# Kernel tuning notes

Hardware: AMD Instinct MI355X
Metric: run time of the kernel (lower is better)

The kernel has to match this reference:

```python
import jax, jax.numpy as jnp
import numpy as np
import math

B, S, D, H, DK, FF, L = 4, 1024, 512, 8, 64, 2048, 4
IN, NS, SD, TOPK = 768, 4, 64, 2


def _ln(x, g, b, eps=1e-5):
    mu = jnp.mean(x, -1, keepdims=True)
    var = jnp.mean((x - mu) ** 2, -1, keepdims=True)
    return (x - mu) / jnp.sqrt(var + eps) * g + b


def _pos_emb(s, d):
    pos = jnp.arange(s, dtype=jnp.float32)[:, None]
    div = jnp.exp(jnp.arange(0, d, 2, dtype=jnp.float32) * (-math.log(10000.0) / d))
    pe = jnp.zeros((s, d), jnp.float32)
    pe = pe.at[:, 0::2].set(jnp.sin(pos * div))
    pe = pe.at[:, 1::2].set(jnp.cos(pos * div))
    return pe


def setup_inputs() -> dict:
    key = jax.random.key(0)
    ks = iter(jax.random.split(key, 40))
    r = lambda *sh: jax.random.normal(next(ks), sh, jnp.float32)
    p = lambda *sh: jax.random.normal(next(ks), sh, jnp.float32) * 0.02
    inp = {
        'q_raw_seq': r(B, S, NS, IN),
        'm_seq': r(B, S, SD),
        'qa_embed': r(B, S, D),
        # MoE expert FFNs: Linear(IN,IN) -> ReLU -> Linear(IN,D)
        'exp_w1': p(NS, IN, IN), 'exp_b1': jnp.zeros((NS, IN)),
        'exp_w2': p(NS, IN, D), 'exp_b2': jnp.zeros((NS, D)),
        # router input adapter Linear(NS*IN, D)
        'adapt_w': p(NS * IN, D), 'adapt_b': jnp.zeros((D,)),
        'gate_w': p(D + SD, NS), 'gate_b': jnp.zeros((NS,)),
        'moe_ln_g': jnp.ones((D,)), 'moe_ln_b': jnp.zeros((D,)),
        # transformer blocks (kq_same=1 -> k_linear shared for q and k)
        'kw': p(L, D, D), 'kb': jnp.zeros((L, D)),
        'vw': p(L, D, D), 'vb': jnp.zeros((L, D)),
        'ow': p(L, D, D), 'ob': jnp.zeros((L, D)),
        'ln1_g': jnp.ones((L, D)), 'ln1_b': jnp.zeros((L, D)),
        'ff_w1': p(L, D, FF), 'ff_b1': jnp.zeros((L, FF)),
        'ff_w2': p(L, FF, D), 'ff_b2': jnp.zeros((L, D)),
        'ln2_g': jnp.ones((L, D)), 'ln2_b': jnp.zeros((L, D)),
    }
    return inp


def _forward(q_raw_seq, m_seq, qa_embed, exp_w1, exp_b1, exp_w2, exp_b2,
             adapt_w, adapt_b, gate_w, gate_b, moe_ln_g, moe_ln_b,
             kw, kb, vw, vb, ow, ob, ln1_g, ln1_b,
             ff_w1, ff_b1, ff_w2, ff_b2, ln2_g, ln2_b):
    # ---- PolyaParallelMoE (eval: no noise/dropout), has_stages=True ----
    h1 = jax.nn.relu(jnp.einsum('bske,kef->bskf', q_raw_seq, exp_w1) + exp_b1[None, None])
    experts = jnp.einsum('bskf,kfm->bskm', h1, exp_w2) + exp_b2[None, None]  # [B,S,4,D]
    q_flat = q_raw_seq.reshape(q_raw_seq.shape[0], q_raw_seq.shape[1], NS * IN)
    summary = jax.nn.relu(q_flat @ adapt_w + adapt_b)
    logits = jnp.concatenate([summary, m_seq], -1) @ gate_w + gate_b  # [B,S,4]
    top_vals, _ = jax.lax.top_k(logits, TOPK)
    thresh = top_vals[..., -1:]
    masked = jnp.where(logits >= thresh, logits, -jnp.inf)  # scatter top-k, -inf elsewhere
    gate_weights = jax.nn.softmax(masked, -1)
    combined = jnp.einsum('bskm,bsk->bsm', experts, gate_weights)
    q_embed = _ln(combined, moe_ln_g, moe_ln_b)

    # ---- Architecture: positional add + causal transformer blocks ----
    pe = _pos_emb(S, D)
    x = q_embed + pe
    y = qa_embed + pe
    allow = jnp.tril(jnp.ones((S, S), bool), -1)  # strict lower: np.triu(k=0)==0
    scale = 1.0 / math.sqrt(DK)
    for i in range(L):
        kh = (x @ kw[i] + kb[i]).reshape(B, S, H, DK).transpose(0, 2, 1, 3)
        vh = (y @ vw[i] + vb[i]).reshape(B, S, H, DK).transpose(0, 2, 1, 3)
        # kq_same: q = k_linear(query), query==key==x -> qh == kh
        scores = jnp.einsum('bhid,bhjd->bhij', kh, kh) * scale
        scores = jnp.where(allow, scores, -1e32)
        attn = jax.nn.softmax(scores, -1)
        attn = attn.at[:, :, 0, :].set(0.0)  # zero_pad first query row
        ctx = jnp.einsum('bhij,bhjd->bhid', attn, vh).transpose(0, 2, 1, 3).reshape(B, S, D)
        x = _ln(x + (ctx @ ow[i] + ob[i]), ln1_g[i], ln1_b[i])
        ffn = jax.nn.relu(x @ ff_w1[i] + ff_b1[i]) @ ff_w2[i] + ff_b2[i]
        x = _ln(x + ffn, ln2_g[i], ln2_b[i])
        y = x  # after first block, value stream follows torch loop (values=y fixed)
        y = qa_embed + pe  # values stay qa stream per Architecture.forward
    return x


def reference(q_raw_seq, m_seq, qa_embed, exp_w1, exp_b1, exp_w2, exp_b2,
              adapt_w, adapt_b, gate_w, gate_b, moe_ln_g, moe_ln_b,
              kw, kb, vw, vb, ow, ob, ln1_g, ln1_b,
              ff_w1, ff_b1, ff_w2, ff_b2, ln2_g, ln2_b):
    # NOTE: in Architecture.forward, each block is called with query=x, key=x, values=y
    # where y = qa_embed + pe stays fixed across blocks.
    def fwd(*a):
        return _forward(*a)
    return fwd(q_raw_seq, m_seq, qa_embed, exp_w1, exp_b1, exp_w2, exp_b2,
               adapt_w, adapt_b, gate_w, gate_b, moe_ln_g, moe_ln_b,
               kw, kb, vw, vb, ow, ob, ln1_g, ln1_b,
               ff_w1, ff_b1, ff_w2, ff_b2, ln2_g, ln2_b)
```

## Files before the change

kernel.cpp:

```cpp
#include <hip/hip_runtime.h>
#include <hip/hip_bf16.h>

typedef unsigned short u16;
typedef __attribute__((ext_vector_type(8))) short short8;
typedef __attribute__((ext_vector_type(4))) float floatx4;

template <typename T> struct is_u16 { static constexpr bool v = false; };
template <> struct is_u16<u16> { static constexpr bool v = true; };

__device__ __forceinline__ float bf2f(u16 u) {
    unsigned x = (unsigned)u << 16;
    return __uint_as_float(x);
}
__device__ __forceinline__ u16 f2bf(float f) {
    unsigned x = __float_as_uint(f);
    unsigned r = (x + 0x7fffu + ((x >> 16) & 1u)) >> 16;
    return (u16)r;
}

__device__ __forceinline__ float wave_sum(float v) {
    #pragma unroll
    for (int off = 32; off; off >>= 1) v += __shfl_xor(v, off);
    return v;
}

__device__ __forceinline__ void async16(const u16* g, const u16* lds) {
    __builtin_amdgcn_global_load_lds(
        (const __attribute__((address_space(1))) void*)g,
        (__attribute__((address_space(3))) void*)lds, 16, 0, 0);
}

__device__ __forceinline__ void load8f(const float* p, u16* dst) {
    float4 a = *(const float4*)p, b = *(const float4*)(p + 4);
    dst[0] = f2bf(a.x); dst[1] = f2bf(a.y); dst[2] = f2bf(a.z); dst[3] = f2bf(a.w);
    dst[4] = f2bf(b.x); dst[5] = f2bf(b.y); dst[6] = f2bf(b.z); dst[7] = f2bf(b.w);
}

__device__ __forceinline__ void hilo8(const float* p, u16* hi, u16* lo) {
    float4 a = *(const float4*)p, b = *(const float4*)(p + 4);
    float v[8] = {a.x, a.y, a.z, a.w, b.x, b.y, b.z, b.w};
    #pragma unroll
    for (int i = 0; i < 8; ++i) {
        u16 h = f2bf(v[i]);
        hi[i] = h;
        lo[i] = f2bf(v[i] - bf2f(h));
    }
}

__global__ __launch_bounds__(256) void hilo_conv_kernel(
    const float* __restrict__ in, u16* __restrict__ hi, u16* __restrict__ lo)
{
    const size_t i = ((size_t)blockIdx.x * 256 + threadIdx.x) * 8;
    u16 h[8], l[8];
    hilo8(in + i, h, l);
    *(uint4*)&hi[i] = *(const uint4*)h;
    *(uint4*)&lo[i] = *(const uint4*)l;
}

template <typename TA>
__device__ __forceinline__ void gemm_body(
    const TA* __restrict__ A, int lda,
    const u16* __restrict__ Bt, int ldb,
    const float* __restrict__ bias,
    float* __restrict__ Cf, u16* __restrict__ Cb, int ldc,
    int K, int act, int transC)
{
    __shared__ __align__(16) u16 Asm[2 * 128 * 32];
    __shared__ __align__(16) u16 Bsm[2 * 128 * 32];

    const int tid = threadIdx.x;
    const int lane = tid & 63;
    const int wave = tid >> 6;
    const int m0 = blockIdx.y * 128, n0 = blockIdx.x * 128;
    const int wm = (wave >> 1) * 64, wn = (wave & 1) * 64;

    const int r0 = tid >> 2;
    const int kc = (tid & 3) * 8;

    const int kq = (lane >> 4) * 8;
    const int fm = lane & 15;

    const floatx4 zz = {0.f, 0.f, 0.f, 0.f};
    floatx4 acc[4][4];
    #pragma unroll
    for (int mt = 0; mt < 4; ++mt)
        #pragma unroll
        for (int nt = 0; nt < 4; ++nt) acc[mt][nt] = zz;

    const u16* ldsA = Asm + wave * 512;
    const u16* ldsB = Bsm + wave * 512;

    for (int kt = 0; kt < K; kt += 64) {
        if constexpr (is_u16<TA>::v) {
            #pragma unroll
            for (int h = 0; h < 2; ++h) {
                async16(&A[(size_t)(m0 + r0) * lda + kt + h * 32 + kc],      ldsA + h * 4096);
                async16(&A[(size_t)(m0 + r0 + 64) * lda + kt + h * 32 + kc], ldsA + h * 4096 + 2048);
                async16(&Bt[(size_t)(n0 + r0) * ldb + kt + h * 32 + kc],      ldsB + h * 4096);
                async16(&Bt[(size_t)(n0 + r0 + 64) * ldb + kt + h * 32 + kc], ldsB + h * 4096 + 2048);
            }
        } else {
            #pragma unroll
            for (int h = 0; h < 2; ++h) {
                load8f(&A[(size_t)(m0 + r0) * lda + kt + h * 32 + kc],      &Asm[h * 4096 + r0 * 32 + kc]);
                load8f(&A[(size_t)(m0 + r0 + 64) * lda + kt + h * 32 + kc], &Asm[h * 4096 + (r0 + 64) * 32 + kc]);
                *(uint4*)&Bsm[h * 4096 + r0 * 32 + kc]        = *(const uint4*)&Bt[(size_t)(n0 + r0) * ldb + kt + h * 32 + kc];
                *(uint4*)&Bsm[h * 4096 + (r0 + 64) * 32 + kc] = *(const uint4*)&Bt[(size_t)(n0 + r0 + 64) * ldb + kt + h * 32 + kc];
            }
        }
        __syncthreads();

        #pragma unroll
        for (int h = 0; h < 2; ++h) {
            short8 af[4], bfr[4];
            #pragma unroll
            for (int mt = 0; mt < 4; ++mt)
                af[mt] = *(const short8*)&Asm[h * 4096 + (wm + mt * 16 + fm) * 32 + kq];
            #pragma unroll
            for (int nt = 0; nt < 4; ++nt)
                bfr[nt] = *(const short8*)&Bsm[h * 4096 + (wn + nt * 16 + fm) * 32 + kq];

            #pragma unroll
            for (int mt = 0; mt < 4; ++mt)
                #pragma unroll
                for (int nt = 0; nt < 4; ++nt)
                    acc[mt][nt] = __builtin_amdgcn_mfma_f32_16x16x32_bf16(
                        af[mt], bfr[nt], acc[mt][nt], 0, 0, 0);
        }
        __syncthreads();
    }

    const int cr = (lane >> 4) * 4;
    #pragma unroll
    for (int mt = 0; mt < 4; ++mt) {
        #pragma unroll
        for (int nt = 0; nt < 4; ++nt) {
            const int col = n0 + wn + nt * 16 + fm;
            const float bz = bias ? bias[col] : 0.f;
            #pragma unroll
            for (int r = 0; r < 4; ++r) {
                const int row = m0 + wm + mt * 16 + cr + r;
                float v = acc[mt][nt][r] + bz;
                if (act) v = fmaxf(v, 0.f);
                if (Cf) Cf[(size_t)row * ldc + col] = v;
                if (Cb) {
                    if (transC)
                        Cb[(((size_t)(row >> 10) * 512 + col) << 10) + (row & 1023)] = f2bf(v);
                    else
                        Cb[(size_t)row * ldc + col] = f2bf(v);
                }
            }
        }
    }
}

template <typename TA>
__global__ __launch_bounds__(256) void gemm_bf16(
    const TA* __restrict__ A, int lda, long strideAz,
    const u16* __restrict__ Bt, int ldb, long strideBz,
    const float* __restrict__ bias, int strideBiasZ,
    float* __restrict__ Cf, u16* __restrict__ Cb, int ldc, long strideCz,
    int K, int act, int transC)
{
    A += (size_t)blockIdx.z * strideAz;
    Bt += (size_t)blockIdx.z * strideBz;
    if (bias) bias += (size_t)blockIdx.z * strideBiasZ;
    if (Cf) Cf += (size_t)blockIdx.z * strideCz;
    if (Cb) Cb += (size_t)blockIdx.z * strideCz;
    gemm_body<TA>(A, lda, Bt, ldb, bias, Cf, Cb, ldc, K, act, transC);
}

__global__ __launch_bounds__(256) void gemm_kv(
    const u16* __restrict__ xb, const u16* __restrict__ yb,
    const u16* __restrict__ kwt, const u16* __restrict__ vwt,
    const float* __restrict__ kb, const float* __restrict__ vb,
    u16* __restrict__ khb, u16* __restrict__ vhT)
{
    if (blockIdx.z == 0)
        gemm_body<u16>(xb, 512, kwt, 512, kb, nullptr, khb, 512, 512, 0, 0);
    else
        gemm_body<u16>(yb, 512, vwt, 512, vb, nullptr, vhT, 512, 512, 0, 1);
}

__global__ __launch_bounds__(256) void gemm_f32split(
    const u16* __restrict__ Ah, const u16* __restrict__ Al, int lda,
    const u16* __restrict__ Bh, const u16* __restrict__ Bl, int ldb,
    float* __restrict__ Cf, int ldc, long strideCz,
    int kz)
{
    __shared__ __align__(16) u16 Ahs[128 * 32];
    __shared__ __align__(16) u16 Als[128 * 32];
    __shared__ __align__(16) u16 Bhs[128 * 32];
    __shared__ __align__(16) u16 Bls[128 * 32];

    const int tid = threadIdx.x;
    const int lane = tid & 63;
    const int wave = tid >> 6;
    const int m0 = blockIdx.y * 128, n0 = blockIdx.x * 128;
    const int wm = (wave >> 1) * 64, wn = (wave & 1) * 64;
    const int k0 = blockIdx.z * kz;
    Cf += (size_t)blockIdx.z * strideCz;

    const int r0 = tid >> 2;
    const int kc = (tid & 3) * 8;
    const int kq = (lane >> 4) * 8;
    const int fm = lane & 15;

    const floatx4 zz = {0.f, 0.f, 0.f, 0.f};
    floatx4 acc[4][4];
    #pragma unroll
    for (int mt = 0; mt < 4; ++mt)
        #pragma unroll
        for (int nt = 0; nt < 4; ++nt) acc[mt][nt] = zz;

    const u16* ldsAh0 = Ahs + wave * 512;
    const u16* ldsAh1 = Ahs + 2048 + wave * 512;
    const u16* ldsAl0 = Als + wave * 512;
    const u16* ldsAl1 = Als + 2048 + wave * 512;
    const u16* ldsBh0 = Bhs + wave * 512;
    const u16* ldsBh1 = Bhs + 2048 + wave * 512;
    const u16* ldsBl0 = Bls + wave * 512;
    const u16* ldsBl1 = Bls + 2048 + wave * 512;

    for (int kt = 0; kt < kz; kt += 32) {
        const size_t ka = (size_t)(m0 + r0) * lda + k0 + kt + kc;
        const size_t kb = (size_t)(n0 + r0) * ldb + k0 + kt + kc;
        async16(&Ah[ka],                     ldsAh0);
        async16(&Ah[ka + (size_t)64 * lda],  ldsAh1);
        async16(&Al[ka],                     ldsAl0);
        async16(&Al[ka + (size_t)64 * lda],  ldsAl1);
        async16(&Bh[kb],                     ldsBh0);
        async16(&Bh[kb + (size_t)64 * ldb],  ldsBh1);
        async16(&Bl[kb],                     ldsBl0);
        async16(&Bl[kb + (size_t)64 * ldb],  ldsBl1);
        __syncthreads();

        short8 ah[4], al[4], bh[4], bl[4];
        #pragma unroll
        for (int mt = 0; mt < 4; ++mt) {
            ah[mt] = *(const short8*)&Ahs[(wm + mt * 16 + fm) * 32 + kq];
            al[mt] = *(const short8*)&Als[(wm + mt * 16 + fm) * 32 + kq];
        }
        #pragma unroll
        for (int nt = 0; nt < 4; ++nt) {
            bh[nt] = *(const short8*)&Bhs[(wn + nt * 16 + fm) * 32 + kq];
            bl[nt] = *(const short8*)&Bls[(wn + nt * 16 + fm) * 32 + kq];
        }

        #pragma unroll
        for (int mt = 0; mt < 4; ++mt)
            #pragma unroll
            for (int nt = 0; nt < 4; ++nt) {
                acc[mt][nt] = __builtin_amdgcn_mfma_f32_16x16x32_bf16(
                    ah[mt], bh[nt], acc[mt][nt], 0, 0, 0);
                acc[mt][nt] = __builtin_amdgcn_mfma_f32_16x16x32_bf16(
                    al[mt], bh[nt], acc[mt][nt], 0, 0, 0);
                acc[mt][nt] = __builtin_amdgcn_mfma_f32_16x16x32_bf16(
                    ah[mt], bl[nt], acc[mt][nt], 0, 0, 0);
            }
        __syncthreads();
    }

    const int cr = (lane >> 4) * 4;
    #pragma unroll
    for (int mt = 0; mt < 4; ++mt) {
        #pragma unroll
        for (int nt = 0; nt < 4; ++nt) {
            const int col = n0 + wn + nt * 16 + fm;
            #pragma unroll
            for (int r = 0; r < 4; ++r) {
                const int row = m0 + wm + mt * 16 + cr + r;
                Cf[(size_t)row * ldc + col] = acc[mt][nt][r];
            }
        }
    }
}

__global__ __launch_bounds__(64) void gate_fused_kernel(
    const float* __restrict__ ps, const float* __restrict__ adapt_b,
    const float* __restrict__ m_seq,
    const float* __restrict__ gw, const float* __restrict__ gb,
    float* __restrict__ gates)
{
    const int r = blockIdx.x, t = threadIdx.x;
    float p0 = 0.f, p1 = 0.f, p2 = 0.f, p3 = 0.f;
    const float* pr = ps + (size_t)r * 512;
    for (int j = t; j < 512; j += 64) {
        float v = pr[j] + pr[j + 2097152] + pr[j + 4194304] + pr[j + 6291456] + adapt_b[j];
        float s = fmaxf(v, 0.f);
        const float* g = gw + (size_t)j * 4;
        p0 += s * g[0]; p1 += s * g[1]; p2 += s * g[2]; p3 += s * g[3];
    }
    {
        float m = m_seq[(size_t)r * 64 + t];
        const float* g = gw + (size_t)(512 + t) * 4;
        p0 += m * g[0]; p1 += m * g[1]; p2 += m * g[2]; p3 += m * g[3];
    }
    p0 = wave_sum(p0); p1 = wave_sum(p1); p2 = wave_sum(p2); p3 = wave_sum(p3);
    if (t == 0) {
        float lg[4] = { p0 + gb[0], p1 + gb[1], p2 + gb[2], p3 + gb[3] };
        float m1 = -INFINITY, m2 = -INFINITY;
        #pragma unroll
        for (int k = 0; k < 4; ++k) {
            float v = lg[k];
            if (v > m1) { m2 = m1; m1 = v; }
            else if (v > m2) { m2 = v; }
        }
        float wv[4], s = 0.f;
        #pragma unroll
        for (int k = 0; k < 4; ++k) {
            wv[k] = (lg[k] >= m2) ? __expf(lg[k] - m1) : 0.f;
            s += wv[k];
        }
        float inv = 1.f / s;
        #pragma unroll
        for (int k = 0; k < 4; ++k) gates[(size_t)r * 4 + k] = wv[k] * inv;
    }
}

__global__ __launch_bounds__(256) void tconv_kernel(
    const float* __restrict__ in, u16* __restrict__ out, int K, int N)
{
    __shared__ float t[32][33];
    const int n0 = blockIdx.x * 32, k0 = blockIdx.y * 32;
    const size_t bo = (size_t)blockIdx.z * K * N;
    const int tx = threadIdx.x & 31, ty = threadIdx.x >> 5;
    const float* src = in + bo;
    u16* dst = out + bo;
    #pragma unroll
    for (int r = ty; r < 32; r += 8) t[r][tx] = src[(size_t)(k0 + r) * N + n0 + tx];
    __syncthreads();
    #pragma unroll
    for (int r = ty; r < 32; r += 8) dst[(size_t)(n0 + r) * K + k0 + tx] = f2bf(t[tx][r]);
}

__global__ __launch_bounds__(256) void tconv3_kernel(
    const float* __restrict__ kw, const float* __restrict__ vw, const float* __restrict__ ow,
    u16* __restrict__ kwt, u16* __restrict__ vwt, u16* __restrict__ owt)
{
    __shared__ float t[32][33];
    const int z = blockIdx.z;
    const int sel = z >> 2, li = z & 3;
    const float* in = (sel == 0) ? kw : (sel == 1) ? vw : ow;
    u16* outp = (sel == 0) ? kwt : (sel == 1) ? vwt : owt;
    const size_t bo = (size_t)li * 262144;
    const int n0 = blockIdx.x * 32, k0 = blockIdx.y * 32;
    const int tx = threadIdx.x & 31, ty = threadIdx.x >> 5;
    const float* src = in + bo;
    u16* dst = outp + bo;
    #pragma unroll
    for (int r = ty; r < 32; r += 8) t[r][tx] = src[(size_t)(k0 + r) * 512 + n0 + tx];
    __syncthreads();
    #pragma unroll
    for (int r = ty; r < 32; r += 8) dst[(size_t)(n0 + r) * 512 + k0 + tx] = f2bf(t[tx][r]);
}

__global__ __launch_bounds__(256) void tconv_hilo_kernel(
    const float* __restrict__ in, u16* __restrict__ outh, u16* __restrict__ outl,
    int K, int N)
{
    __shared__ float t[32][33];
    const int n0 = blockIdx.x * 32, k0 = blockIdx.y * 32;
    const int tx = threadIdx.x & 31, ty = threadIdx.x >> 5;
    #pragma unroll
    for (int r = ty; r < 32; r += 8) t[r][tx] = in[(size_t)(k0 + r) * N + n0 + tx];
    __syncthreads();
    #pragma unroll
    for (int r = ty; r < 32; r += 8) {
        float v = t[tx][r];
        u16 h = f2bf(v);
        outh[(size_t)(n0 + r) * K + k0 + tx] = h;
        outl[(size_t)(n0 + r) * K + k0 + tx] = f2bf(v - bf2f(h));
    }
}

__global__ void pe_kernel(float* __restrict__ pe)
{
    int idx = blockIdx.x * 256 + threadIdx.x;
    int s = idx >> 9, d = idx & 511;
    float div = expf((float)(d & ~1) * (-9.210340371976184f / 512.0f));
    float ang = (float)s * div;
    pe[idx] = (d & 1) ? cosf(ang) : sinf(ang);
}

__global__ __launch_bounds__(64) void moe_ln_kernel(
    const u16* __restrict__ experts, const float* __restrict__ gates,
    const float* __restrict__ g, const float* __restrict__ bb,
    const float* __restrict__ pe, const float* __restrict__ qa,
    float* __restrict__ x, u16* __restrict__ xb, u16* __restrict__ yb)
{
    const int r = blockIdx.x, t = threadIdx.x;
    const u16* e = experts + (size_t)r * 2048;
    const float g0 = gates[r * 4 + 0], g1 = gates[r * 4 + 1];
    const float g2 = gates[r * 4 + 2], g3 = gates[r * 4 + 3];
    float v[8];
    #pragma unroll
    for (int it = 0; it < 8; ++it) {
        int d = t + it * 64;
        v[it] = g0 * bf2f(e[d]) + g1 * bf2f(e[512 + d])
              + g2 * bf2f(e[1024 + d]) + g3 * bf2f(e[1536 + d]);
    }
    float s = 0.f;
    #pragma unroll
    for (int it = 0; it < 8; ++it) s += v[it];
    s = wave_sum(s);
    const float mu = s * (1.f / 512.f);
    float q = 0.f;
    #pragma unroll
    for (int it = 0; it < 8; ++it) { float dd = v[it] - mu; q += dd * dd; }
    q = wave_sum(q);
    const float rstd = rsqrtf(q * (1.f / 512.f) + 1e-5f);
    const float* per = pe + (size_t)(r & 1023) * 512;
    #pragma unroll
    for (int it = 0; it < 8; ++it) {
        int d = t + it * 64;
        float pv = per[d];
        float o = (v[it] - mu) * rstd * g[d] + bb[d] + pv;
        x[(size_t)r * 512 + d] = o;
        xb[(size_t)r * 512 + d] = f2bf(o);
        yb[(size_t)r * 512 + d] = f2bf(qa[(size_t)r * 512 + d] + pv);
    }
}

__global__ __launch_bounds__(64) void add_ln_kernel(
    float* __restrict__ x, u16* __restrict__ xb,
    const float* __restrict__ t0, const float* __restrict__ t1,
    const float* __restrict__ bias,
    const float* __restrict__ g, const float* __restrict__ bb,
    float* __restrict__ out2)
{
    const int r = blockIdx.x, t = threadIdx.x;
    float* xr = x + (size_t)r * 512;
    float v[8];
    #pragma unroll
    for (int it = 0; it < 8; ++it) {
        int d = t + it * 64;
        float tv = t0[(size_t)r * 512 + d];
        if (t1) tv += t1[(size_t)r * 512 + d];
        if (bias) tv += bias[d];
        v[it] = xr[d] + tv;
    }
    float s = 0.f;
    #pragma unroll
    for (int it = 0; it < 8; ++it) s += v[it];
    s = wave_sum(s);
    const float mu = s * (1.f / 512.f);
    float q = 0.f;
    #pragma unroll
    for (int it = 0; it < 8; ++it) { float dd = v[it] - mu; q += dd * dd; }
    q = wave_sum(q);
    const float rstd = rsqrtf(q * (1.f / 512.f) + 1e-5f);
    #pragma unroll
    for (int it = 0; it < 8; ++it) {
        int d = t + it * 64;
        float o = (v[it] - mu) * rstd * g[d] + bb[d];
        xr[d] = o;
        xb[(size_t)r * 512 + d] = f2bf(o);
        if (out2) out2[(size_t)r * 512 + d] = o;
    }
}

__global__ __launch_bounds__(256) void attn_kernel(
    const u16* __restrict__ kh, const u16* __restrict__ vhT,
    u16* __restrict__ ctx)
{
    __shared__ __align__(16) u16 Qs[64 * 64];
    __shared__ __align__(16) u16 Ks[64 * 64];
    __shared__ __align__(16) u16 Vt[64 * 72];
    __shared__ __align__(16) u16 Ps[64 * 72];

    const int tid = threadIdx.x;
    const int lane = tid & 63, wave = tid >> 6;
    const int quad = lane >> 4, fm = lane & 15;
    const int b = blockIdx.x, h = blockIdx.y;
    const int bz = blockIdx.z;
    const int it = (bz < 8) ? bz : (23 - bz);

    const u16* khb = kh + ((size_t)b * 1024) * 512 + h * 64;
    const u16* vtb = vhT + ((size_t)(b * 512 + h * 64)) * 1024;

    const int lj = tid >> 2;
    const int lc = tid & 3;

    {
        const u16* src = khb + (size_t)(it * 64 + lj) * 512 + lc * 16;
        *(uint4*)&Qs[lj * 64 + lc * 16]     = *(const uint4*)src;
        *(uint4*)&Qs[lj * 64 + lc * 16 + 8] = *(const uint4*)(src + 8);
    }

    const floatx4 zz = {0.f, 0.f, 0.f, 0.f};
    floatx4 o_acc[4];
    #pragma unroll
    for (int nt = 0; nt < 4; ++nt) o_acc[nt] = zz;
    float m_run[4] = { -INFINITY, -INFINITY, -INFINITY, -INFINITY };
    float l_run[4] = {};

    __syncthreads();

    for (int jt = 0; jt <= it; ++jt) {
        {
            const u16* ksrc = khb + (size_t)(jt * 64 + lj) * 512 + lc * 16;
            *(uint4*)&Ks[lj * 64 + lc * 16]     = *(const uint4*)ksrc;
            *(uint4*)&Ks[lj * 64 + lc * 16 + 8] = *(const uint4*)(ksrc + 8);
            const u16* vsrc = vtb + (size_t)lj * 1024 + jt * 64 + lc * 16;
            *(uint4*)&Vt[lj * 72 + lc * 16]     = *(const uint4*)vsrc;
            *(uint4*)&Vt[lj * 72 + lc * 16 + 8] = *(const uint4*)(vsrc + 8);
        }
        __syncthreads();

        floatx4 s_acc[4];
        #pragma unroll
        for (int nt = 0; nt < 4; ++nt) s_acc[nt] = zz;
        #pragma unroll
        for (int ks = 0; ks < 2; ++ks) {
            short8 af = *(const short8*)&Qs[(wave * 16 + fm) * 64 + ks * 32 + quad * 8];
            #pragma unroll
            for (int nt = 0; nt < 4; ++nt) {
                short8 bf = *(const short8*)&Ks[(nt * 16 + fm) * 64 + ks * 32 + quad * 8];
                s_acc[nt] = __builtin_amdgcn_mfma_f32_16x16x32_bf16(af, bf, s_acc[nt], 0, 0, 0);
            }
        }

        const bool diag = (jt == it);
        #pragma unroll
        for (int r = 0; r < 4; ++r) {
            const int rowi = wave * 16 + quad * 4 + r;
            float sv[4];
            #pragma unroll
            for (int nt = 0; nt < 4; ++nt) {
                float s = s_acc[nt][r] * 0.125f;
                if (diag && (nt * 16 + fm) >= rowi) s = -INFINITY;
                sv[nt] = s;
            }
            float mx = fmaxf(fmaxf(sv[0], sv[1]), fmaxf(sv[2], sv[3]));
            #pragma unroll
            for (int off = 1; off < 16; off <<= 1) mx = fmaxf(mx, __shfl_xor(mx, off));
            const float mn = fmaxf(m_run[r], mx);
            const float mfix = (mn == -INFINITY) ? 0.f : mn;
            const float alpha = (m_run[r] == -INFINITY) ? 0.f : __expf(m_run[r] - mn);
            m_run[r] = mn;
            float rs = 0.f;
            #pragma unroll
            for (int nt = 0; nt < 4; ++nt) {
                float p = __expf(sv[nt] - mfix);
                Ps[rowi * 72 + nt * 16 + fm] = f2bf(p);
                rs += p;
            }
            #pragma unroll
            for (int off = 1; off < 16; off <<= 1) rs += __shfl_xor(rs, off);
            l_run[r] = l_run[r] * alpha + rs;
            #pragma unroll
            for (int nt = 0; nt < 4; ++nt) o_acc[nt][r] *= alpha;
        }
        __syncthreads();

        #pragma unroll
        for (int ks = 0; ks < 2; ++ks) {
            short8 af = *(const short8*)&Ps[(wave * 16 + fm) * 72 + ks * 32 + quad * 8];
            #pragma unroll
            for (int nt = 0; nt < 4; ++nt) {
                short8 bf = *(const short8*)&Vt[(nt * 16 + fm) * 72 + ks * 32 + quad * 8];
                o_acc[nt] = __builtin_amdgcn_mfma_f32_16x16x32_bf16(af, bf, o_acc[nt], 0, 0, 0);
            }
        }
        __syncthreads();
    }

    u16* cb = ctx + ((size_t)b * 1024 + (size_t)it * 64 + wave * 16) * 512 + h * 64;
    #pragma unroll
    for (int r = 0; r < 4; ++r) {
        const int row = quad * 4 + r;
        const float inv = (l_run[r] > 0.f) ? 1.f / l_run[r] : 0.f;
        #pragma unroll
        for (int nt = 0; nt < 4; ++nt)
            cb[(size_t)row * 512 + nt * 16 + fm] = f2bf(o_acc[nt][r] * inv);
    }
}

extern "C" void kernel_launch(void* const* d_in, const int* in_sizes, int n_in,
                              void* d_out, int out_size, void* d_ws, size_t ws_size,
                              hipStream_t stream)
{
    const float* q_raw   = (const float*)d_in[0];
    const float* m_seq   = (const float*)d_in[1];
    const float* qa      = (const float*)d_in[2];
    const float* exp_w1  = (const float*)d_in[3];
    const float* exp_b1  = (const float*)d_in[4];
    const float* exp_w2  = (const float*)d_in[5];
    const float* exp_b2  = (const float*)d_in[6];
    const float* adapt_w = (const float*)d_in[7];
    const float* adapt_b = (const float*)d_in[8];
    const float* gate_w  = (const float*)d_in[9];
    const float* gate_b  = (const float*)d_in[10];
    const float* moe_g   = (const float*)d_in[11];
    const float* moe_b   = (const float*)d_in[12];
    const float* kw      = (const float*)d_in[13];
    const float* kb      = (const float*)d_in[14];
    const float* vw      = (const float*)d_in[15];
    const float* vb      = (const float*)d_in[16];
    const float* ow      = (const float*)d_in[17];
    const float* ob      = (const float*)d_in[18];
    const float* ln1g    = (const float*)d_in[19];
    const float* ln1b    = (const float*)d_in[20];
    const float* fw1     = (const float*)d_in[21];
    const float* fb1     = (const float*)d_in[22];
    const float* fw2     = (const float*)d_in[23];
    const float* fb2     = (const float*)d_in[24];
    const float* ln2g    = (const float*)d_in[25];
    const float* ln2b    = (const float*)d_in[26];
    float* out = (float*)d_out;

    const size_t NEED = 125829120ull;
    if (ws_size < NEED) return;

    char* base = (char*)d_ws;
    float* x  = (float*)(base + 0);
    u16*  xb  = (u16*)(base + 8388608);
    u16*  yb  = (u16*)(base + 12582912);
    char* G = base + 16777216;
    u16*   w1t     = (u16*)(G + 0);
    u16*   w2t     = (u16*)(G + 4718592);
    float* psum    = (float*)(G + 7864320);
    u16*   h1b4    = (u16*)(G + 7864320);
    u16*   expb    = (u16*)(G + 33030144);
    float* pe      = (float*)(G + 49807360);
    float* gates   = (float*)(G + 51904512);
    u16*   adwh    = (u16*)(G + 52428800);
    u16*   adwl    = (u16*)(G + 55574528);
    u16*   qhi     = (u16*)(G + 58720256);
    u16*   qlo     = (u16*)(G + 83886080);
    u16*   kwt  = (u16*)(G + 0);
    u16*   vwt  = (u16*)(G + 2097152);
    u16*   owt  = (u16*)(G + 4194304);
    u16*   fw1t = (u16*)(G + 6291456);
    u16*   fw2t = (u16*)(G + 14680064);
    u16*   khb  = (u16*)(G + 23068672);
    u16*   vhT  = (u16*)(G + 27262976);
    u16*   ctxb = (u16*)(G + 31457280);
    float* p    = (float*)(G + 35651584);
    u16*   ffhb = (u16*)(G + 44040192);
    float* ps0  = (float*)(G + 23068672);

    pe_kernel<<<2048, 256, 0, stream>>>(pe);
    hilo_conv_kernel<<<6144, 256, 0, stream>>>(q_raw, qhi, qlo);
    tconv_kernel<<<dim3(24, 24, 4), 256, 0, stream>>>(exp_w1, w1t, 768, 768);
    tconv_kernel<<<dim3(16, 24, 4), 256, 0, stream>>>(exp_w2, w2t, 768, 512);
    tconv_hilo_kernel<<<dim3(16, 96), 256, 0, stream>>>(adapt_w, adwh, adwl, 3072, 512);

    gemm_f32split<<<dim3(4, 32, 4), 256, 0, stream>>>(
        qhi, qlo, 3072, adwh, adwl, 3072, psum, 512, 2097152L, 768);
    gate_fused_kernel<<<4096, 64, 0, stream>>>(
        psum, adapt_b, m_seq, gate_w, gate_b, gates);

    gemm_bf16<u16><<<dim3(6, 32, 4), 256, 0, stream>>>(
        qhi, 3072, 768L, w1t, 768, 589824L, exp_b1, 768,
        nullptr, h1b4, 768, 3145728L, 768, 1, 0);
    gemm_bf16<u16><<<dim3(4, 32, 4), 256, 0, stream>>>(
        h1b4, 768, 3145728L, w2t, 768, 393216L, exp_b2, 512,
        nullptr, expb, 2048, 512L, 768, 0, 0);
    moe_ln_kernel<<<4096, 64, 0, stream>>>(expb, gates, moe_g, moe_b, pe, qa, x, xb, yb);

    tconv3_kernel<<<dim3(16, 16, 12), 256, 0, stream>>>(kw, vw, ow, kwt, vwt, owt);
    tconv_kernel<<<dim3(64, 16, 4), 256, 0, stream>>>(fw1, fw1t, 512, 2048);
    tconv_kernel<<<dim3(16, 64, 4), 256, 0, stream>>>(fw2, fw2t, 2048, 512);

    for (int i = 0; i < 4; ++i) {
        gemm_kv<<<dim3(4, 32, 2), 256, 0, stream>>>(
            xb, yb, kwt + (size_t)i * 262144, vwt + (size_t)i * 262144,
            kb + i * 512, vb + i * 512, khb, vhT);
        attn_kernel<<<dim3(4, 8, 16), 256, 0, stream>>>(khb, vhT, ctxb);
        gemm_bf16<u16><<<dim3(4, 32), 256, 0, stream>>>(
            ctxb, 512, 0L, owt + (size_t)i * 262144, 512, 0L, ob + i * 512, 0,
            p, nullptr, 512, 0L, 512, 0, 0);
        add_ln_kernel<<<4096, 64, 0, stream>>>(
            x, xb, p, nullptr, nullptr, ln1g + i * 512, ln1b + i * 512, nullptr);
        gemm_bf16<u16><<<dim3(16, 32), 256, 0, stream>>>(
            xb, 512, 0L, fw1t + (size_t)i * 1048576, 512, 0L, fb1 + i * 2048, 0,
            nullptr, ffhb, 2048, 0L, 512, 1, 0);
        gemm_bf16<u16><<<dim3(4, 32, 2), 256, 0, stream>>>(
            ffhb, 2048, 1024L, fw2t + (size_t)i * 1048576, 2048, 1024L, nullptr, 0,
            ps0, nullptr, 512, 2097152L, 1024, 0, 0);
        add_ln_kernel<<<4096, 64, 0, stream>>>(
            x, xb, ps0, ps0 + 2097152, fb2 + i * 512,
            ln2g + i * 512, ln2b + i * 512, (i == 3) ? out : nullptr);
    }
}
```

Before: 925.8 us.

## Double K-step per barrier and remap split-precision GEMM blocks for XCD locality

The hi/lo split-precision adapter GEMM now loads two 32-wide K slices per iteration into doubled LDS buffers. This halves the number of barrier pairs per tile. The 3D grid becomes a 1D grid of 512 blocks, remapped so that the four N-tiles sharing the same A rows land on the same XCD, which improves L2 reuse of A. LDS use doubles to 64KB per block, which may reduce occupancy.

```diff
diff --git a/kernel.cpp b/kernel.cpp
--- a/kernel.cpp
+++ b/kernel.cpp
@@ -188,18 +188,25 @@
     float* __restrict__ Cf, int ldc, long strideCz,
     int kz)
 {
-    __shared__ __align__(16) u16 Ahs[128 * 32];
-    __shared__ __align__(16) u16 Als[128 * 32];
-    __shared__ __align__(16) u16 Bhs[128 * 32];
-    __shared__ __align__(16) u16 Bls[128 * 32];
+    __shared__ __align__(16) u16 Ahs[2 * 128 * 32];
+    __shared__ __align__(16) u16 Als[2 * 128 * 32];
+    __shared__ __align__(16) u16 Bhs[2 * 128 * 32];
+    __shared__ __align__(16) u16 Bls[2 * 128 * 32];
+
+    const int wg   = blockIdx.x;
+    const int xcd  = wg & 7;
+    const int slot = wg >> 3;
+    const int nt4  = slot & 3;
+    const int g    = xcd + 8 * (slot >> 2);
+    const int my   = g & 31, mz = g >> 5;
 
     const int tid = threadIdx.x;
     const int lane = tid & 63;
     const int wave = tid >> 6;
-    const int m0 = blockIdx.y * 128, n0 = blockIdx.x * 128;
+    const int m0 = my * 128, n0 = nt4 * 128;
     const int wm = (wave >> 1) * 64, wn = (wave & 1) * 64;
-    const int k0 = blockIdx.z * kz;
-    Cf += (size_t)blockIdx.z * strideCz;
+    const int k0 = mz * kz;
+    Cf += (size_t)mz * strideCz;
 
     const int r0 = tid >> 2;
     const int kc = (tid & 3) * 8;
@@ -213,51 +220,53 @@
         #pragma unroll
         for (int nt = 0; nt < 4; ++nt) acc[mt][nt] = zz;
 
-    const u16* ldsAh0 = Ahs + wave * 512;
-    const u16* ldsAh1 = Ahs + 2048 + wave * 512;
-    const u16* ldsAl0 = Als + wave * 512;
-    const u16* ldsAl1 = Als + 2048 + wave * 512;
-    const u16* ldsBh0 = Bhs + wave * 512;
-    const u16* ldsBh1 = Bhs + 2048 + wave * 512;
-    const u16* ldsBl0 = Bls + wave * 512;
-    const u16* ldsBl1 = Bls + 2048 + wave * 512;
-
-    for (int kt = 0; kt < kz; kt += 32) {
-        const size_t ka = (size_t)(m0 + r0) * lda + k0 + kt + kc;
-        const size_t kb = (size_t)(n0 + r0) * ldb + k0 + kt + kc;
-        async16(&Ah[ka],                     ldsAh0);
-        async16(&Ah[ka + (size_t)64 * lda],  ldsAh1);
-        async16(&Al[ka],                     ldsAl0);
-        async16(&Al[ka + (size_t)64 * lda],  ldsAl1);
-        async16(&Bh[kb],                     ldsBh0);
-        async16(&Bh[kb + (size_t)64 * ldb],  ldsBh1);
-        async16(&Bl[kb],                     ldsBl0);
-        async16(&Bl[kb + (size_t)64 * ldb],  ldsBl1);
+    const u16* ldsAh = Ahs + wave * 512;
+    const u16* ldsAl = Als + wave * 512;
+    const u16* ldsBh = Bhs + wave * 512;
+    const u16* ldsBl = Bls + wave * 512;
+
+    for (int kt = 0; kt < kz; kt += 64) {
+        #pragma unroll
+        for (int h = 0; h < 2; ++h) {
+            const size_t ka = (size_t)(m0 + r0) * lda + k0 + kt + h * 32 + kc;
+            const size_t kb = (size_t)(n0 + r0) * ldb + k0 + kt + h * 32 + kc;
+            async16(&Ah[ka],                     ldsAh + h * 4096);
+            async16(&Ah[ka + (size_t)64 * lda],  ldsAh + h * 4096 + 2048);
+            async16(&Al[ka],                     ldsAl + h * 4096);
+            async16(&Al[ka + (size_t)64 * lda],  ldsAl + h * 4096 + 2048);
+            async16(&Bh[kb],                     ldsBh + h * 4096);
+            async16(&Bh[kb + (size_t)64 * ldb],  ldsBh + h * 4096 + 2048);
+            async16(&Bl[kb],                     ldsBl + h * 4096);
+            async16(&Bl[kb + (size_t)64 * ldb],  ldsBl + h * 4096 + 2048);
+        }
         __syncthreads();
 
-        short8 ah[4], al[4], bh[4], bl[4];
-        #pragma unroll
-        for (int mt = 0; mt < 4; ++mt) {
-            ah[mt] = *(const short8*)&Ahs[(wm + mt * 16 + fm) * 32 + kq];
-            al[mt] = *(const short8*)&Als[(wm + mt * 16 + fm) * 32 + kq];
-        }
-        #pragma unroll
-        for (int nt = 0; nt < 4; ++nt) {
-            bh[nt] = *(const short8*)&Bhs[(wn + nt * 16 + fm) * 32 + kq];
-            bl[nt] = *(const short8*)&Bls[(wn + nt * 16 + fm) * 32 + kq];
-        }
-
-        #pragma unroll
-        for (int mt = 0; mt < 4; ++mt)
+        #pragma unroll
+        for (int h = 0; h < 2; ++h) {
+            short8 ah[4], al[4], bh[4], bl[4];
+            #pragma unroll
+            for (int mt = 0; mt < 4; ++mt) {
+                ah[mt] = *(const short8*)&Ahs[h * 4096 + (wm + mt * 16 + fm) * 32 + kq];
+                al[mt] = *(const short8*)&Als[h * 4096 + (wm + mt * 16 + fm) * 32 + kq];
+            }
             #pragma unroll
             for (int nt = 0; nt < 4; ++nt) {
-                acc[mt][nt] = __builtin_amdgcn_mfma_f32_16x16x32_bf16(
-                    ah[mt], bh[nt], acc[mt][nt], 0, 0, 0);
-                acc[mt][nt] = __builtin_amdgcn_mfma_f32_16x16x32_bf16(
-                    al[mt], bh[nt], acc[mt][nt], 0, 0, 0);
-                acc[mt][nt] = __builtin_amdgcn_mfma_f32_16x16x32_bf16(
-                    ah[mt], bl[nt], acc[mt][nt], 0, 0, 0);
-            }
+                bh[nt] = *(const short8*)&Bhs[h * 4096 + (wn + nt * 16 + fm) * 32 + kq];
+                bl[nt] = *(const short8*)&Bls[h * 4096 + (wn + nt * 16 + fm) * 32 + kq];
+            }
+
+            #pragma unroll
+            for (int mt = 0; mt < 4; ++mt)
+                #pragma unroll
+                for (int nt = 0; nt < 4; ++nt) {
+                    acc[mt][nt] = __builtin_amdgcn_mfma_f32_16x16x32_bf16(
+                        ah[mt], bh[nt], acc[mt][nt], 0, 0, 0);
+                    acc[mt][nt] = __builtin_amdgcn_mfma_f32_16x16x32_bf16(
+                        al[mt], bh[nt], acc[mt][nt], 0, 0, 0);
+                    acc[mt][nt] = __builtin_amdgcn_mfma_f32_16x16x32_bf16(
+                        ah[mt], bl[nt], acc[mt][nt], 0, 0, 0);
+                }
+        }
         __syncthreads();
     }
 
@@ -647,7 +656,7 @@
     tconv_kernel<<<dim3(16, 24, 4), 256, 0, stream>>>(exp_w2, w2t, 768, 512);
     tconv_hilo_kernel<<<dim3(16, 96), 256, 0, stream>>>(adapt_w, adwh, adwl, 3072, 512);
 
-    gemm_f32split<<<dim3(4, 32, 4), 256, 0, stream>>>(
+    gemm_f32split<<<512, 256, 0, stream>>>(
         qhi, qlo, 3072, adwh, adwl, 3072, psum, 512, 2097152L, 768);
     gate_fused_kernel<<<4096, 64, 0, stream>>>(
         psum, adapt_b, m_seq, gate_w, gate_b, gates);
```

New measurement: 916.5 us. No clear change (-1.0%).
